# Kernel optimization log

Measured on AMD Instinct MI355X. Metric: run time of the kernel, lower is better.

## Reference

```python
import jax, jax.numpy as jnp
import numpy as np
import math

BS, QLEN, DIM, NHEADS = 2, 2048, 1024, 16
DPH = DIM // NHEADS


def setup_inputs() -> dict:
    key = jax.random.key(0)
    ks = jax.random.split(key, 10)
    s = 0.02
    return {
        "input": jax.random.normal(ks[0], (BS, QLEN, DIM), jnp.float32),
        "mask": jax.random.randint(ks[1], (BS, QLEN), 0, 2, jnp.int32),
        "Wq": jax.random.normal(ks[2], (DIM, DIM), jnp.float32) * s,
        "bq": jnp.zeros((DIM,), jnp.float32),
        "Wk": jax.random.normal(ks[3], (DIM, DIM), jnp.float32) * s,
        "bk": jnp.zeros((DIM,), jnp.float32),
        "Wv": jax.random.normal(ks[4], (DIM, DIM), jnp.float32) * s,
        "bv": jnp.zeros((DIM,), jnp.float32),
        "Wo": jax.random.normal(ks[5], (DIM, DIM), jnp.float32) * s,
        "bo": jnp.zeros((DIM,), jnp.float32),
    }


def _shape(x):
    # (bs, len, dim) -> (bs, heads, len, dph)
    return x.reshape(BS, -1, NHEADS, DPH).transpose(0, 2, 1, 3)


def reference(input, mask, Wq, bq, Wk, bk, Wv, bv, Wo, bo):
    q = _shape(input @ Wq.T + bq)
    k = _shape(input @ Wk.T + bk)
    v = _shape(input @ Wv.T + bv)
    q = q / math.sqrt(DPH)
    scores = jnp.einsum("bhqd,bhkd->bhqk", q, k)  # (bs, h, qlen, klen)
    # original masked_fill_ with 1e-10 (NOT -inf)
    m = (mask == 0)[:, None, None, :]  # (bs,1,1,klen)
    scores = jnp.where(m, jnp.float32(1e-10), scores)
    weights = jax.nn.softmax(scores.astype(jnp.float32), axis=-1).astype(scores.dtype)
    # dropout p=0.0 / eval mode -> identity
    context = jnp.einsum("bhqk,bhkd->bhqd", weights, v)
    context = context.transpose(0, 2, 1, 3).reshape(BS, -1, DIM)
    return context @ Wo.T + bo
```

## Files before the change

### kernel.cpp

```cpp
#include <hip/hip_runtime.h>

typedef __attribute__((ext_vector_type(8))) _Float16 half8;
typedef __attribute__((ext_vector_type(4))) _Float16 half4;
typedef __attribute__((ext_vector_type(4))) float f32x4;
typedef __attribute__((ext_vector_type(16))) float f32x16;
typedef __attribute__((ext_vector_type(4))) int int4v;

#define BS 2
#define QLEN 2048
#define DIM 1024
#define NH 16
#define DPH 64
#define MTOT (BS * QLEN)
#define LOG2E 1.44269504088896340736f

#define WAITB(N)                                          \
    asm volatile("s_waitcnt vmcnt(" #N ")" ::: "memory"); \
    __builtin_amdgcn_s_barrier();                         \
    __builtin_amdgcn_sched_barrier(0)
#define ENDB()                                            \
    __builtin_amdgcn_sched_barrier(0);                    \
    __builtin_amdgcn_s_barrier()

__global__ void cvt_all(const float* __restrict__ x,
                        const float* __restrict__ wq, const float* __restrict__ wk,
                        const float* __restrict__ wv, const float* __restrict__ wo,
                        _Float16* __restrict__ X16,
                        _Float16* __restrict__ Wq16, _Float16* __restrict__ Wk16,
                        _Float16* __restrict__ Wv16, _Float16* __restrict__ Wo16) {
    const int NX = (MTOT * DIM) / 4;
    const int NW = (DIM * DIM) / 4;
    const int total = NX + 4 * NW;
    int idx = blockIdx.x * blockDim.x + threadIdx.x;
    int stride = gridDim.x * blockDim.x;
    for (int i = idx; i < total; i += stride) {
        const float* src; _Float16* dst; int off;
        if (i < NX) { src = x; dst = X16; off = i; }
        else {
            int k = i - NX; int which = k / NW; off = k - which * NW;
            src = which == 0 ? wq : which == 1 ? wk : which == 2 ? wv : wo;
            dst = which == 0 ? Wq16 : which == 1 ? Wk16 : which == 2 ? Wv16 : Wo16;
        }
        float4 v = ((const float4*)src)[off];
        half4 o;
        o[0] = (_Float16)v.x; o[1] = (_Float16)v.y;
        o[2] = (_Float16)v.z; o[3] = (_Float16)v.w;
        ((half4*)dst)[off] = o;
    }
}

__device__ __forceinline__ void gload_lds16(const _Float16* g, _Float16* l) {
    __builtin_amdgcn_global_load_lds(
        (const __attribute__((address_space(1))) void*)g,
        (__attribute__((address_space(3))) void*)l, 16, 0, 0);
}

__global__ __launch_bounds__(256) void gemm_qkv(
    const _Float16* __restrict__ A,
    const _Float16* __restrict__ Wq, const _Float16* __restrict__ Wk,
    const _Float16* __restrict__ Wv,
    const float* __restrict__ bq, const float* __restrict__ bk,
    const float* __restrict__ bv, const int* __restrict__ mask,
    _Float16* __restrict__ Qd, _Float16* __restrict__ Kd,
    _Float16* __restrict__ Vd) {
    const int K = 1024;
    __shared__ _Float16 sA[2][128 * 32];
    __shared__ _Float16 sB[2][128 * 32];

    const int flat = blockIdx.x;
    const int xcd = flat & 7, seq = flat >> 3;
    const int ya = xcd >> 1, nb = xcd & 1;
    const int n_hi = seq & 3;
    const int rem = seq >> 2;
    const int z = rem % 3, y_hi = rem / 3;
    const int y = y_hi * 4 + ya;
    const int nblk = n_hi * 2 + nb;
    const int m0 = y * 128, n0 = nblk * 128;

    const _Float16* W = (z == 0) ? Wq : (z == 1) ? Wk : Wv;
    const float* bias = (z == 0) ? bq : (z == 1) ? bk : bv;

    const int tid = threadIdx.x, w = tid >> 6, l = tid & 63;
    const int wr = (w >> 1) * 64, wc = (w & 1) * 64;
    const int r = l & 15, g = l >> 4;

    const _Float16* gA[2];
    const _Float16* gW[2];
    _Float16* dA[2];
    _Float16* dB[2];
#pragma unroll
    for (int i = 0; i < 2; ++i) {
        int s = tid + i * 256, row = s >> 2, pos = s & 3;
        int chunk = pos ^ (row & 3);
        gA[i] = &A[(size_t)(m0 + row) * K + chunk * 8];
        gW[i] = &W[(size_t)(n0 + row) * K + chunk * 8];
        dA[i] = &sA[0][s * 8];
        dB[i] = &sB[0][s * 8];
    }
    auto stageAdv = [&](int bb) {
#pragma unroll
        for (int i = 0; i < 2; ++i) {
            gload_lds16(gA[i], dA[i] + bb * 4096);
            gload_lds16(gW[i], dB[i] + bb * 4096);
            gA[i] += 32;
            gW[i] += 32;
        }
    };

    const int fpos = (g ^ (r & 3)) * 8;
    const _Float16* pA[4];
    const _Float16* pB[4];
#pragma unroll
    for (int i = 0; i < 4; ++i) {
        pA[i] = &sA[0][(wr + i * 16 + r) * 32] + fpos;
        pB[i] = &sB[0][(wc + i * 16 + r) * 32] + fpos;
    }

    f32x4 acc[4][4] = {};
    auto compute = [&](int bb) {
        const int boff = bb * 4096;
        half8 af[4], bf[4];
#pragma unroll
        for (int i = 0; i < 4; ++i) {
            af[i] = *(const half8*)(pA[i] + boff);
            bf[i] = *(const half8*)(pB[i] + boff);
        }
#pragma unroll
        for (int i = 0; i < 4; ++i)
#pragma unroll
            for (int j = 0; j < 4; ++j)
                acc[i][j] = __builtin_amdgcn_mfma_f32_16x16x32_f16(
                    af[i], bf[j], acc[i][j], 0, 0, 0);
    };

    stageAdv(0);
    for (int t = 0; t < 16; ++t) {
        stageAdv(1);
        WAITB(4);
        compute(0);
        ENDB();
        stageAdv(0);
        WAITB(4);
        compute(1);
        ENDB();
    }

    float bv4[4];
#pragma unroll
    for (int j = 0; j < 4; ++j) bv4[j] = bias[n0 + wc + j * 16 + r];

#pragma unroll
    for (int i = 0; i < 4; ++i)
#pragma unroll
        for (int j = 0; j < 4; ++j) {
            const int n = n0 + wc + j * 16 + r;
            const int h = n >> 6, d = n & 63;
#pragma unroll
            for (int reg = 0; reg < 4; ++reg) {
                const int m = m0 + wr + i * 16 + g * 4 + reg;
                const int bb = m >> 11, tt = m & 2047;
                float v = acc[i][j][reg] + bv4[j];
                if (z == 0)
                    Qd[(((size_t)(bb * NH + h)) * QLEN + tt) * DPH + d] =
                        (_Float16)(v * (0.125f * LOG2E));
                else if (z == 1) {
                    v = mask[bb * QLEN + tt] ? v : 0.f;
                    Kd[(((size_t)(bb * NH + h)) * QLEN + tt) * DPH + d] = (_Float16)v;
                } else
                    Vd[(((size_t)(bb * NH + h)) * DPH + d) * QLEN + tt] = (_Float16)v;
            }
        }
}

__global__ __launch_bounds__(256) void gemm_out(
    const _Float16* __restrict__ A, const _Float16* __restrict__ W,
    const float* __restrict__ bias, float* __restrict__ out) {
    const int K = 1024;
    __shared__ _Float16 sA[2][64 * 32];
    __shared__ _Float16 sB[2][128 * 32];
    const int m0 = blockIdx.y * 64, n0 = blockIdx.x * 128;
    const int tid = threadIdx.x, w = tid >> 6, l = tid & 63;
    const int wr = (w >> 1) * 32, wc = (w & 1) * 64;
    const int r = l & 15, g = l >> 4;

    const _Float16* gA;
    const _Float16* gB[2];
    _Float16* dA;
    _Float16* dB[2];
    {
        int s = tid, row = s >> 2, seg = (s & 3) * 8;
        gA = &A[(size_t)(m0 + row) * K + seg];
        dA = &sA[0][s * 8];
    }
#pragma unroll
    for (int i = 0; i < 2; ++i) {
        int s = tid + i * 256, row = s >> 2, seg = (s & 3) * 8;
        gB[i] = &W[(size_t)(n0 + row) * K + seg];
        dB[i] = &sB[0][s * 8];
    }
    auto stageAdv = [&](int bb) {
        gload_lds16(gA, dA + bb * 2048);
        gA += 32;
#pragma unroll
        for (int i = 0; i < 2; ++i) {
            gload_lds16(gB[i], dB[i] + bb * 4096);
            gB[i] += 32;
        }
    };

    const _Float16* pA[2];
    const _Float16* pB[4];
#pragma unroll
    for (int i = 0; i < 2; ++i)
        pA[i] = &sA[0][(wr + i * 16 + r) * 32 + g * 8];
#pragma unroll
    for (int j = 0; j < 4; ++j)
        pB[j] = &sB[0][(wc + j * 16 + r) * 32 + g * 8];

    f32x4 acc[2][4] = {};
    auto compute = [&](int bb) {
        half8 af[2], bf[4];
#pragma unroll
        for (int i = 0; i < 2; ++i)
            af[i] = *(const half8*)(pA[i] + bb * 2048);
#pragma unroll
        for (int j = 0; j < 4; ++j)
            bf[j] = *(const half8*)(pB[j] + bb * 4096);
#pragma unroll
        for (int i = 0; i < 2; ++i)
#pragma unroll
            for (int j = 0; j < 4; ++j)
                acc[i][j] = __builtin_amdgcn_mfma_f32_16x16x32_f16(
                    af[i], bf[j], acc[i][j], 0, 0, 0);
    };

    stageAdv(0);
    for (int t = 0; t < 16; ++t) {
        stageAdv(1);
        WAITB(3);
        compute(0);
        ENDB();
        stageAdv(0);
        WAITB(3);
        compute(1);
        ENDB();
    }

    float bv4[4];
#pragma unroll
    for (int j = 0; j < 4; ++j) bv4[j] = bias[n0 + wc + j * 16 + r];
#pragma unroll
    for (int i = 0; i < 2; ++i)
#pragma unroll
        for (int j = 0; j < 4; ++j) {
            const int n = n0 + wc + j * 16 + r;
#pragma unroll
            for (int reg = 0; reg < 4; ++reg) {
                const int m = m0 + wr + i * 16 + g * 4 + reg;
                out[(size_t)m * DIM + n] = acc[i][j][reg] + bv4[j];
            }
        }
}

__global__ __launch_bounds__(512) void attn_kernel(
    const _Float16* __restrict__ Qg, const _Float16* __restrict__ Kg,
    const _Float16* __restrict__ Vg, _Float16* __restrict__ ctx) {
    __shared__ __align__(16) char smem[65536];

    const int flat = blockIdx.x;
    const int qt = (flat >> 3) & 15;
    const int bh = ((flat >> 7) << 3) | (flat & 7);
    const int b = bh >> 4, h = bh & 15;
    const _Float16* __restrict__ Qp = Qg + (size_t)bh * QLEN * DPH;
    const _Float16* __restrict__ Kp = Kg + (size_t)bh * QLEN * DPH;
    const _Float16* __restrict__ Vp = Vg + (size_t)bh * DPH * QLEN;

    const int tid = threadIdx.x, w = tid >> 6, l = tid & 63;
    const int qsub = w & 3, ksplit = w >> 2;
    const int ln = l & 31, hi = l >> 5;
    const int q0 = qt * 128 + qsub * 32;
    const int kbase = ksplit * 1024;

    _Float16* sK0 = (_Float16*)(smem + ksplit * 2 * 8192);
    _Float16* sV0 = (_Float16*)(smem + 32768 + ksplit * 2 * 8192);

    half8 qf[4];
#pragma unroll
    for (int ks = 0; ks < 4; ++ks)
        qf[ks] = *(const half8*)&Qp[(size_t)(q0 + ln) * DPH + ks * 16 + hi * 8];

    f32x16 accT[2] = {};
    float lsum = 0.f;

    const _Float16* kptr[2][4];
    const _Float16* vptr[2][2][2];
#pragma unroll
    for (int kb = 0; kb < 2; ++kb) {
#pragma unroll
        for (int ks = 0; ks < 4; ++ks)
            kptr[kb][ks] = sK0 + (kb * 32 + ln) * 64 + ((ks * 2 + hi) ^ (ln & 7)) * 8;
#pragma unroll
        for (int dblk = 0; dblk < 2; ++dblk) {
            vptr[kb][dblk][0] =
                sV0 + (dblk * 32 + ln) * 64 + ((kb * 4 + 0 + hi) ^ (ln & 7)) * 8;
            vptr[kb][dblk][1] =
                sV0 + (dblk * 32 + ln) * 64 + ((kb * 4 + 2 + hi) ^ (ln & 7)) * 8;
        }
    }

    const int c8 = ((l & 7) ^ (l >> 3)) * 8;
    const int rl = l >> 3;
    const _Float16* gK[2];
    const _Float16* gV[2];
    _Float16* dK[2];
    _Float16* dV[2];
#pragma unroll
    for (int j = 0; j < 2; ++j) {
        const int r0 = qsub * 16 + j * 8;
        gK[j] = &Kp[(size_t)(kbase + r0 + rl) * DPH + c8];
        gV[j] = &Vp[(size_t)(r0 + rl) * QLEN + kbase + c8];
        dK[j] = sK0 + r0 * 64 + l * 8;
        dV[j] = sV0 + r0 * 64 + l * 8;
    }

    auto stageAdv = [&](int bb) {
#pragma unroll
        for (int j = 0; j < 2; ++j) {
            gload_lds16(gK[j], dK[j] + bb * 4096);
            gload_lds16(gV[j], dV[j] + bb * 4096);
            gK[j] += 64 * DPH;
            gV[j] += 64;
        }
    };

    auto compute = [&](int bb) {
        const int boff = bb * 4096;
#pragma unroll
        for (int kb = 0; kb < 2; ++kb) {
            f32x16 st = {};
            __builtin_amdgcn_s_setprio(1);
#pragma unroll
            for (int ks = 0; ks < 4; ++ks) {
                half8 kf = *(const half8*)(kptr[kb][ks] + boff);
                st = __builtin_amdgcn_mfma_f32_32x32x16_f16(kf, qf[ks], st, 0, 0, 0);
            }
            __builtin_amdgcn_s_setprio(0);

            int cpk[8];
#pragma unroll
            for (int i = 0; i < 8; ++i) {
                float e0 = __builtin_amdgcn_exp2f(st[2 * i]);
                float e1 = __builtin_amdgcn_exp2f(st[2 * i + 1]);
                lsum += e0 + e1;
                cpk[i] =
                    __builtin_bit_cast(int, __builtin_amdgcn_cvt_pkrtz(e0, e1));
            }
            asm("v_permlane32_swap_b32 %0, %1" : "+v"(cpk[0]), "+v"(cpk[2]));
            asm("v_permlane32_swap_b32 %0, %1" : "+v"(cpk[1]), "+v"(cpk[3]));
            asm("v_permlane32_swap_b32 %0, %1" : "+v"(cpk[4]), "+v"(cpk[6]));
            asm("v_permlane32_swap_b32 %0, %1" : "+v"(cpk[5]), "+v"(cpk[7]));
            int4v b0 = {cpk[0], cpk[1], cpk[2], cpk[3]};
            int4v b1 = {cpk[4], cpk[5], cpk[6], cpk[7]};
            half8 Bf0 = __builtin_bit_cast(half8, b0);
            half8 Bf1 = __builtin_bit_cast(half8, b1);

            __builtin_amdgcn_s_setprio(1);
#pragma unroll
            for (int dblk = 0; dblk < 2; ++dblk) {
                half8 vf0 = *(const half8*)(vptr[kb][dblk][0] + boff);
                half8 vf1 = *(const half8*)(vptr[kb][dblk][1] + boff);
                accT[dblk] = __builtin_amdgcn_mfma_f32_32x32x16_f16(
                    vf0, Bf0, accT[dblk], 0, 0, 0);
                accT[dblk] = __builtin_amdgcn_mfma_f32_32x32x16_f16(
                    vf1, Bf1, accT[dblk], 0, 0, 0);
            }
            __builtin_amdgcn_s_setprio(0);
        }
    };

    stageAdv(0);
    __syncthreads();
    for (int t = 0; t < 8; ++t) {
        stageAdv(1);
        compute(0);
        __syncthreads();
        stageAdv(0);
        compute(1);
        __syncthreads();
    }

    lsum += __shfl_xor(lsum, 32);

    float* sRed = (float*)smem;
    if (ksplit == 1) {
        float* p = sRed + (qsub * 64 + l) * 33;
#pragma unroll
        for (int dblk = 0; dblk < 2; ++dblk)
#pragma unroll
            for (int i = 0; i < 16; ++i)
                p[dblk * 16 + i] = accT[dblk][i];
        p[32] = lsum;
    }
    __syncthreads();
    if (ksplit == 1) return;

    const float* p = sRed + (qsub * 64 + l) * 33;
#pragma unroll
    for (int dblk = 0; dblk < 2; ++dblk)
#pragma unroll
        for (int i = 0; i < 16; ++i)
            accT[dblk][i] += p[dblk * 16 + i];
    lsum += p[32];

    const float inv = 1.f / lsum;
    _Float16* cp = ctx + ((size_t)(b * QLEN) + q0 + ln) * DIM + h * DPH;
#pragma unroll
    for (int dblk = 0; dblk < 2; ++dblk)
#pragma unroll
        for (int j = 0; j < 4; ++j) {
            half4 o4;
#pragma unroll
            for (int e = 0; e < 4; ++e)
                o4[e] = (_Float16)(accT[dblk][4 * j + e] * inv);
            *(half4*)&cp[dblk * 32 + 8 * j + 4 * hi] = o4;
        }
}

extern "C" void kernel_launch(void* const* d_in, const int* in_sizes, int n_in,
                              void* d_out, int out_size, void* d_ws, size_t ws_size,
                              hipStream_t stream) {
    const float* x  = (const float*)d_in[0];
    const int* mask = (const int*)d_in[1];
    const float* Wq = (const float*)d_in[2];
    const float* bq = (const float*)d_in[3];
    const float* Wk = (const float*)d_in[4];
    const float* bk = (const float*)d_in[5];
    const float* Wv = (const float*)d_in[6];
    const float* bv = (const float*)d_in[7];
    const float* Wo = (const float*)d_in[8];
    const float* bo = (const float*)d_in[9];
    float* out = (float*)d_out;

    char* ws = (char*)d_ws;
    const size_t MB = 1u << 20;
    _Float16* X16  = (_Float16*)(ws + 0);
    _Float16* Wq16 = (_Float16*)(ws + 8 * MB);
    _Float16* Wk16 = (_Float16*)(ws + 10 * MB);
    _Float16* Wv16 = (_Float16*)(ws + 12 * MB);
    _Float16* Wo16 = (_Float16*)(ws + 14 * MB);
    _Float16* Q16  = (_Float16*)(ws + 16 * MB);
    _Float16* K16  = (_Float16*)(ws + 24 * MB);
    _Float16* V16T = (_Float16*)(ws + 32 * MB);
    _Float16* CTX  = (_Float16*)(ws + 40 * MB);

    cvt_all<<<2048, 256, 0, stream>>>(x, Wq, Wk, Wv, Wo,
                                      X16, Wq16, Wk16, Wv16, Wo16);

    gemm_qkv<<<768, 256, 0, stream>>>(
        X16, Wq16, Wk16, Wv16, bq, bk, bv, mask, Q16, K16, V16T);

    attn_kernel<<<512, 512, 0, stream>>>(Q16, K16, V16T, CTX);

    gemm_out<<<dim3(8, 64), 256, 0, stream>>>(CTX, Wo16, bo, out);
}
```

Baseline: 119.1 us.

## Use 2-wave blocks with 64x128 warp tiles in QKV GEMM, drop LDS swizzle

The QKV projection GEMM now launches 128-thread blocks (2 waves) instead of 4 waves. Each wave computes a 64x128 output tile (4x8 MFMA fragments) instead of 64x64, which raises the reuse of each A fragment loaded from LDS. Each thread now issues 4 global-to-LDS loads per operand per stage, and the XOR swizzle of LDS chunk positions is removed. In exchange, accumulator register pressure doubles and LDS bank conflicts may increase without the swizzle, and there are fewer waves per block to hide latency.

```diff
diff --git a/kernel.cpp b/kernel.cpp
--- a/kernel.cpp
+++ b/kernel.cpp
@@ -55,7 +55,7 @@
         (__attribute__((address_space(3))) void*)l, 16, 0, 0);
 }
 
-__global__ __launch_bounds__(256) void gemm_qkv(
+__global__ __launch_bounds__(128) void gemm_qkv(
     const _Float16* __restrict__ A,
     const _Float16* __restrict__ Wq, const _Float16* __restrict__ Wk,
     const _Float16* __restrict__ Wv,
@@ -81,25 +81,25 @@
     const float* bias = (z == 0) ? bq : (z == 1) ? bk : bv;
 
     const int tid = threadIdx.x, w = tid >> 6, l = tid & 63;
-    const int wr = (w >> 1) * 64, wc = (w & 1) * 64;
+    const int wr = w * 64;
     const int r = l & 15, g = l >> 4;
 
-    const _Float16* gA[2];
-    const _Float16* gW[2];
-    _Float16* dA[2];
-    _Float16* dB[2];
-#pragma unroll
-    for (int i = 0; i < 2; ++i) {
-        int s = tid + i * 256, row = s >> 2, pos = s & 3;
-        int chunk = pos ^ (row & 3);
-        gA[i] = &A[(size_t)(m0 + row) * K + chunk * 8];
-        gW[i] = &W[(size_t)(n0 + row) * K + chunk * 8];
+    const _Float16* gA[4];
+    const _Float16* gW[4];
+    _Float16* dA[4];
+    _Float16* dB[4];
+#pragma unroll
+    for (int i = 0; i < 4; ++i) {
+        int s = tid + i * 128;
+        int row = s >> 2, seg = (s & 3) * 8;
+        gA[i] = &A[(size_t)(m0 + row) * K + seg];
+        gW[i] = &W[(size_t)(n0 + row) * K + seg];
         dA[i] = &sA[0][s * 8];
         dB[i] = &sB[0][s * 8];
     }
     auto stageAdv = [&](int bb) {
 #pragma unroll
-        for (int i = 0; i < 2; ++i) {
+        for (int i = 0; i < 4; ++i) {
             gload_lds16(gA[i], dA[i] + bb * 4096);
             gload_lds16(gW[i], dB[i] + bb * 4096);
             gA[i] += 32;
@@ -107,28 +107,29 @@
         }
     };
 
-    const int fpos = (g ^ (r & 3)) * 8;
     const _Float16* pA[4];
-    const _Float16* pB[4];
-#pragma unroll
-    for (int i = 0; i < 4; ++i) {
-        pA[i] = &sA[0][(wr + i * 16 + r) * 32] + fpos;
-        pB[i] = &sB[0][(wc + i * 16 + r) * 32] + fpos;
-    }
-
-    f32x4 acc[4][4] = {};
+    const _Float16* pB[8];
+#pragma unroll
+    for (int i = 0; i < 4; ++i)
+        pA[i] = &sA[0][(wr + i * 16 + r) * 32 + g * 8];
+#pragma unroll
+    for (int j = 0; j < 8; ++j)
+        pB[j] = &sB[0][(j * 16 + r) * 32 + g * 8];
+
+    f32x4 acc[4][8] = {};
     auto compute = [&](int bb) {
         const int boff = bb * 4096;
-        half8 af[4], bf[4];
-#pragma unroll
-        for (int i = 0; i < 4; ++i) {
+        half8 af[4], bf[8];
+#pragma unroll
+        for (int i = 0; i < 4; ++i)
             af[i] = *(const half8*)(pA[i] + boff);
-            bf[i] = *(const half8*)(pB[i] + boff);
-        }
+#pragma unroll
+        for (int j = 0; j < 8; ++j)
+            bf[j] = *(const half8*)(pB[j] + boff);
 #pragma unroll
         for (int i = 0; i < 4; ++i)
 #pragma unroll
-            for (int j = 0; j < 4; ++j)
+            for (int j = 0; j < 8; ++j)
                 acc[i][j] = __builtin_amdgcn_mfma_f32_16x16x32_f16(
                     af[i], bf[j], acc[i][j], 0, 0, 0);
     };
@@ -136,30 +137,30 @@
     stageAdv(0);
     for (int t = 0; t < 16; ++t) {
         stageAdv(1);
-        WAITB(4);
+        WAITB(8);
         compute(0);
         ENDB();
         stageAdv(0);
-        WAITB(4);
+        WAITB(8);
         compute(1);
         ENDB();
     }
 
-    float bv4[4];
-#pragma unroll
-    for (int j = 0; j < 4; ++j) bv4[j] = bias[n0 + wc + j * 16 + r];
+    float bv8[8];
+#pragma unroll
+    for (int j = 0; j < 8; ++j) bv8[j] = bias[n0 + j * 16 + r];
 
 #pragma unroll
     for (int i = 0; i < 4; ++i)
 #pragma unroll
-        for (int j = 0; j < 4; ++j) {
-            const int n = n0 + wc + j * 16 + r;
+        for (int j = 0; j < 8; ++j) {
+            const int n = n0 + j * 16 + r;
             const int h = n >> 6, d = n & 63;
 #pragma unroll
             for (int reg = 0; reg < 4; ++reg) {
                 const int m = m0 + wr + i * 16 + g * 4 + reg;
                 const int bb = m >> 11, tt = m & 2047;
-                float v = acc[i][j][reg] + bv4[j];
+                float v = acc[i][j][reg] + bv8[j];
                 if (z == 0)
                     Qd[(((size_t)(bb * NH + h)) * QLEN + tt) * DPH + d] =
                         (_Float16)(v * (0.125f * LOG2E));
@@ -456,7 +457,7 @@
     cvt_all<<<2048, 256, 0, stream>>>(x, Wq, Wk, Wv, Wo,
                                       X16, Wq16, Wk16, Wv16, Wo16);
 
-    gemm_qkv<<<768, 256, 0, stream>>>(
+    gemm_qkv<<<768, 128, 0, stream>>>(
         X16, Wq16, Wk16, Wv16, bq, bk, bv, mask, Q16, K16, V16T);
 
     attn_kernel<<<512, 512, 0, stream>>>(Q16, K16, V16T, CTX);
```

New measurement: 153.5 us. 28.9% more time.
